# Kernel optimization log

Measured on AMD Instinct MI355X. Metric: run time of the kernel, lower is better.

The kernel has to match this reference:

```python
import jax, jax.numpy as jnp
import numpy as np

HH, WW = 56, 56          # input resolution
WS, SS = 7, 3            # window size, shift size
HEADS = 6
DIM = 192
HID = 768
B = 32
EPS = 1e-5


def _rel_pos_index(ws):
    coords = np.stack(np.meshgrid(np.arange(ws), np.arange(ws), indexing='ij'))  # [2,ws,ws]
    cf = coords.reshape(2, -1)                       # [2,N]
    rel = cf[:, :, None] - cf[:, None, :]            # [2,N,N]
    rel = rel.transpose(1, 2, 0).copy()              # [N,N,2]
    rel[:, :, 0] += ws - 1
    rel[:, :, 1] += ws - 1
    rel[:, :, 0] *= 2 * ws - 1
    return rel.sum(-1)                               # [N,N] int


def _attn_mask(H, W, ws, ss):
    img = np.zeros((H, W))
    cnt = 0
    sl = (slice(0, -ws), slice(-ws, -ss), slice(-ss, None))
    for hs in sl:
        for wsl in sl:
            img[hs, wsl] = cnt
            cnt += 1
    mw = img.reshape(H // ws, ws, W // ws, ws).transpose(0, 2, 1, 3).reshape(-1, ws * ws)  # [nW,N]
    diff = mw[:, None, :] - mw[:, :, None]           # matches unsqueeze(1)-unsqueeze(2)
    return np.where(diff != 0, -100.0, 0.0).astype(np.float32)  # [nW,N,N]


_RPI = jnp.asarray(_rel_pos_index(WS))               # [49,49] int
_MASK = jnp.asarray(_attn_mask(HH, WW, WS, SS))      # [64,49,49] f32


def _ln(v, g, b):
    mu = v.mean(-1, keepdims=True)
    var = v.var(-1, keepdims=True)
    return (v - mu) / jnp.sqrt(var + EPS) * g + b


def setup_inputs() -> dict:
    key = jax.random.key(0)
    ks = jax.random.split(key, 10)
    s = 0.02
    return {
        'x': jax.random.normal(ks[0], (B, HH * WW, DIM), jnp.float32),
        'norm1_g': jnp.ones((DIM,), jnp.float32),
        'norm1_b': jnp.zeros((DIM,), jnp.float32),
        'qkv_w': jax.random.normal(ks[1], (DIM, 3 * DIM), jnp.float32) * s,
        'qkv_b': jax.random.normal(ks[2], (3 * DIM,), jnp.float32) * s,
        'rpb_table': jax.random.normal(ks[3], (169, HEADS), jnp.float32) * s,
        'proj_w': jax.random.normal(ks[4], (DIM, DIM), jnp.float32) * s,
        'proj_b': jax.random.normal(ks[5], (DIM,), jnp.float32) * s,
        'norm2_g': jnp.ones((DIM,), jnp.float32),
        'norm2_b': jnp.zeros((DIM,), jnp.float32),
        'fc1_w': jax.random.normal(ks[6], (DIM, HID), jnp.float32) * s,
        'fc1_b': jax.random.normal(ks[7], (HID,), jnp.float32) * s,
        'fc2_w': jax.random.normal(ks[8], (HID, DIM), jnp.float32) * s,
        'fc2_b': jax.random.normal(ks[9], (DIM,), jnp.float32) * s,
    }


def reference(x, norm1_g, norm1_b, qkv_w, qkv_b, rpb_table, proj_w, proj_b,
              norm2_g, norm2_b, fc1_w, fc1_b, fc2_w, fc2_b):
    Bn, L, C = x.shape
    h, ws, ss = HEADS, WS, SS
    d = C // h
    scale = d ** -0.5
    N = ws * ws
    nWh, nWw = HH // ws, WW // ws

    shortcut = x
    xh = _ln(x, norm1_g, norm1_b).reshape(Bn, HH, WW, C)
    xh = jnp.roll(xh, (-ss, -ss), axis=(1, 2))                       # cyclic shift
    # window partition -> (B*nW, N, C)
    xw = xh.reshape(Bn, nWh, ws, nWw, ws, C).transpose(0, 1, 3, 2, 4, 5).reshape(-1, N, C)

    qkv = (xw @ qkv_w + qkv_b).reshape(-1, N, 3, h, d).transpose(2, 0, 3, 1, 4)
    q, k, v = qkv[0] * scale, qkv[1], qkv[2]                         # (B_,h,N,d)
    attn = jnp.einsum('bhnd,bhmd->bhnm', q, k)                       # (B_,h,N,N)

    bias = rpb_table[_RPI.reshape(-1)].reshape(N, N, h).transpose(2, 0, 1)  # (h,N,N)
    attn = attn + bias[None]
    nW = _MASK.shape[0]
    attn = attn.reshape(Bn, nW, h, N, N) + _MASK[None, :, None]
    attn = jax.nn.softmax(attn.reshape(-1, h, N, N), axis=-1)

    out = jnp.einsum('bhnm,bhmd->bhnd', attn, v).transpose(0, 2, 1, 3).reshape(-1, N, C)
    out = out @ proj_w + proj_b
    # window reverse
    out = out.reshape(Bn, nWh, nWw, ws, ws, C).transpose(0, 1, 3, 2, 4, 5).reshape(Bn, HH, WW, C)
    out = jnp.roll(out, (ss, ss), axis=(1, 2)).reshape(Bn, L, C)     # reverse shift

    x1 = shortcut + out
    y = _ln(x1, norm2_g, norm2_b)
    y = jax.nn.gelu(y @ fc1_w + fc1_b, approximate=False)
    y = y @ fc2_w + fc2_b
    return x1 + y
```

## Files before the change

### kernel.cpp

```cpp
#include <hip/hip_runtime.h>
#include <cmath>

typedef __bf16  v8bf  __attribute__((ext_vector_type(8)));
typedef float   v4f   __attribute__((ext_vector_type(4)));

#define HH 56
#define WW2 56
#define SS 3
#define HEADS 6
#define DIM 192
#define HID 768
#define NTOK 49
#define NWIN 2048
#define MTOT (NWIN * NTOK)
#define SCALE 0.17677669529663687f

__device__ __forceinline__ void async_cp16(const __bf16* g, __bf16* l) {
    __builtin_amdgcn_global_load_lds(
        (const __attribute__((address_space(1))) void*)g,
        (__attribute__((address_space(3))) void*)l,
        16, 0, 0);
}

__global__ void k_transpose(const float* __restrict__ in, __bf16* __restrict__ out,
                            int K, int N) {
    int idx = blockIdx.x * 256 + threadIdx.x;
    if (idx >= K * N) return;
    int n = idx / K, k = idx - n * K;
    out[idx] = (__bf16)in[k * N + n];
}

__global__ void k_prep_fc1(const float* __restrict__ w, __bf16* __restrict__ o) {
    int idx = blockIdx.x * 256 + threadIdx.x;
    if (idx >= HID * DIM) return;
    int n = idx / DIM, rem = idx - n * DIM;
    int b16 = rem >> 3, j = rem & 7;
    int k = 8 * (b16 ^ (n & 7)) + j;
    o[idx] = (__bf16)w[k * HID + n];
}

__global__ void k_prep_fc2(const float* __restrict__ w, __bf16* __restrict__ o) {
    int idx = blockIdx.x * 256 + threadIdx.x;
    if (idx >= HID * DIM) return;
    int hc = idx / (DIM * 64);
    int rem = idx - hc * DIM * 64;
    int n = rem >> 6;
    int rem2 = rem & 63;
    int b16 = rem2 >> 3, j = rem2 & 7;
    int k = hc * 64 + 8 * (b16 ^ (n & 7)) + j;
    o[idx] = (__bf16)w[k * DIM + n];
}

__global__ void k_bias(const float* __restrict__ rpb, float* __restrict__ bt) {
    int type = blockIdx.x, h = blockIdx.y;
    for (int idx = threadIdx.x; idx < 4096; idx += 256) {
        int m = idx >> 6, n = idx & 63;
        float v;
        if (m >= 49) v = -1e9f;
        else if (n >= 49) v = 0.f;
        else {
            int ni = n / 7, nj = n % 7, mi = m / 7, mj = m % 7;
            v = rpb[((ni - mi + 6) * 13 + (nj - mj + 6)) * 6 + h];
            int rin = (type & 2) ? ((ni < 4) ? 1 : 2) : 0;
            int rjn = (type & 1) ? ((nj < 4) ? 1 : 2) : 0;
            int rim = (type & 2) ? ((mi < 4) ? 1 : 2) : 0;
            int rjm = (type & 1) ? ((mj < 4) ? 1 : 2) : 0;
            if (rin * 3 + rjn != rim * 3 + rjm) v -= 100.f;
        }
        bt[((size_t)(type * HEADS + h) * 64 + m) * 64 + n] = v;
    }
}

__global__ __launch_bounds__(256) void k_ln1win(const float* __restrict__ x,
                                                const float* __restrict__ g,
                                                const float* __restrict__ bt,
                                                __bf16* __restrict__ xw) {
    int wv = threadIdx.x >> 6, lane = threadIdx.x & 63;
    int t = blockIdx.x * 4 + wv;
    int w = t / NTOK, p = t - w * NTOK;
    int b = w >> 6, wi = w & 63;
    int i = (wi >> 3) * 7 + p / 7;
    int j = (wi & 7) * 7 + p % 7;
    int io = i + SS; if (io >= HH) io -= HH;
    int jo = j + SS; if (jo >= WW2) jo -= WW2;
    const float* src = x + ((size_t)(b * 3136 + io * 56 + jo)) * DIM;
    float v0 = src[lane], v1 = src[lane + 64], v2 = src[lane + 128];
    float s = v0 + v1 + v2, s2 = v0 * v0 + v1 * v1 + v2 * v2;
    #pragma unroll
    for (int off = 1; off < 64; off <<= 1) {
        s  += __shfl_xor(s, off);
        s2 += __shfl_xor(s2, off);
    }
    float mu = s * (1.f / 192.f);
    float rstd = rsqrtf(s2 * (1.f / 192.f) - mu * mu + 1e-5f);
    __bf16* dst = xw + (size_t)t * DIM;
    dst[lane]       = (__bf16)((v0 - mu) * rstd * g[lane]       + bt[lane]);
    dst[lane + 64]  = (__bf16)((v1 - mu) * rstd * g[lane + 64]  + bt[lane + 64]);
    dst[lane + 128] = (__bf16)((v2 - mu) * rstd * g[lane + 128] + bt[lane + 128]);
}

template<int KDIM, int NDIM, int MODE>
__global__ __launch_bounds__(256) void k_gemm128(const __bf16* __restrict__ A,
                                                 const __bf16* __restrict__ Wt,
                                                 const float* __restrict__ bias,
                                                 __bf16* __restrict__ outb,
                                                 const float* __restrict__ x1in,
                                                 float* __restrict__ outf,
                                                 const float* __restrict__ xres) {
    __shared__ __bf16 lA[128 * 32];
    __shared__ __bf16 lB[128 * 32];
    const int tid = threadIdx.x;
    const int m0 = blockIdx.x * 128, n0 = blockIdx.y * 128;
    const int wv = tid >> 6, lane = tid & 63;
    const int wm = (wv >> 1) * 64, wn = (wv & 1) * 64;
    const int lrow = lane & 15, lq = lane >> 4;
    const int grow = tid >> 2, gkc = (tid & 3) * 8;
    v4f acc[4][4] = {};
    for (int kk = 0; kk < KDIM; kk += 32) {
        #pragma unroll
        for (int c = 0; c < 2; c++) {
            int r = grow + c * 64;
            async_cp16(A + (size_t)(m0 + r) * KDIM + kk + gkc, lA + tid * 8 + c * 2048);
            int rb = n0 + r;
            if (NDIM % 128) rb = (rb < NDIM) ? rb : (NDIM - 1);
            async_cp16(Wt + (size_t)rb * KDIM + kk + gkc, lB + tid * 8 + c * 2048);
        }
        __syncthreads();
        v8bf af[4], bf[4];
        #pragma unroll
        for (int i = 0; i < 4; i++) {
            af[i] = *(const v8bf*)(lA + (wm + i * 16 + lrow) * 32 + lq * 8);
            bf[i] = *(const v8bf*)(lB + (wn + i * 16 + lrow) * 32 + lq * 8);
        }
        #pragma unroll
        for (int i = 0; i < 4; i++)
        #pragma unroll
        for (int j = 0; j < 4; j++)
            acc[i][j] = __builtin_amdgcn_mfma_f32_16x16x32_bf16(af[i], bf[j], acc[i][j], 0, 0, 0);
        __syncthreads();
    }
    #pragma unroll
    for (int i = 0; i < 4; i++)
    #pragma unroll
    for (int j = 0; j < 4; j++) {
        int col = n0 + wn + j * 16 + lrow;
        if (NDIM % 128 && col >= NDIM) continue;
        float bv = bias[col];
        #pragma unroll
        for (int r = 0; r < 4; r++) {
            int row = m0 + wm + i * 16 + lq * 4 + r;
            float v = acc[i][j][r] + bv;
            if (MODE == 0) {
                __bf16* kbp = outb + (size_t)MTOT * DIM;
                __bf16* vbp = kbp + (size_t)MTOT * DIM;
                int which = col / DIM, rem = col - which * DIM;
                int hh = rem >> 5, d = rem & 31;
                int w = row / NTOK, p = row - w * NTOK;
                size_t off = ((size_t)(w * HEADS + hh) * NTOK + p) * 32 + d;
                if (which == 0)      outb[off] = (__bf16)(v * SCALE);
                else if (which == 1) kbp[off] = (__bf16)v;
                else                 vbp[off] = (__bf16)v;
            } else {
                int w = row / NTOK, p = row - w * NTOK;
                int bimg = w >> 6, wi = w & 63;
                int ii = (wi >> 3) * 7 + p / 7;
                int jj = (wi & 7) * 7 + p % 7;
                int io = ii + SS; if (io >= HH) io -= HH;
                int jo = jj + SS; if (jo >= WW2) jo -= WW2;
                size_t o = ((size_t)(bimg * 3136 + io * 56 + jo)) * DIM + col;
                outf[o] = v + xres[o];
            }
        }
    }
}

__global__ __launch_bounds__(64) void k_attn_mfma(const __bf16* __restrict__ qb,
                                                  const float* __restrict__ bias_tab,
                                                  __bf16* __restrict__ ao) {
    __shared__ __bf16 Pl[64 * 72];
    __shared__ __bf16 VTl[32 * 72];
    const __bf16* kb = qb + (size_t)MTOT * DIM;
    const __bf16* vb = kb + (size_t)MTOT * DIM;
    int wh = blockIdx.x;
    int w = wh / HEADS, h = wh - w * HEADS;
    int lane = threadIdx.x & 63;
    int c = lane & 15, q = lane >> 4;
    const size_t base = (size_t)wh * (NTOK * 32);

    for (int idx = lane; idx < 32 * 16; idx += 64)
        VTl[(idx >> 4) * 72 + 48 + (idx & 15)] = (__bf16)0.f;
    #pragma unroll
    for (int it = 0; it < 4; it++) {
        int idx = it * 64 + lane;
        if (idx < NTOK * 4) {
            int t = idx >> 2, d0 = (idx & 3) * 8;
            v8bf vv = *(const v8bf*)(vb + base + t * 32 + d0);
            #pragma unroll
            for (int ii = 0; ii < 8; ii++) VTl[(d0 + ii) * 72 + t] = vv[ii];
        }
    }
    v8bf af[4], bf[4];
    #pragma unroll
    for (int rt = 0; rt < 4; rt++) {
        int t = rt * 16 + c; t = (t > 48) ? 48 : t;
        af[rt] = *(const v8bf*)(qb + base + t * 32 + q * 8);
        bf[rt] = *(const v8bf*)(kb + base + t * 32 + q * 8);
    }
    v4f S[4][4] = {};
    #pragma unroll
    for (int rt = 0; rt < 4; rt++)
    #pragma unroll
    for (int ct = 0; ct < 4; ct++)
        S[rt][ct] = __builtin_amdgcn_mfma_f32_16x16x32_bf16(af[rt], bf[ct], S[rt][ct], 0, 0, 0);
    int wi = w & 63;
    int type = (((wi >> 3) == 7) ? 2 : 0) + (((wi & 7) == 7) ? 1 : 0);
    const float* bt = bias_tab + (size_t)(type * HEADS + h) * 4096;
    #pragma unroll
    for (int rt = 0; rt < 4; rt++)
    #pragma unroll
    for (int ct = 0; ct < 4; ct++) {
        v4f bv = *(const v4f*)(bt + (ct * 16 + c) * 64 + rt * 16 + q * 4);
        S[rt][ct] += bv;
    }
    v4f mx4[4], inv4[4];
    #pragma unroll
    for (int rt = 0; rt < 4; rt++) {
        v4f m;
        #pragma unroll
        for (int r = 0; r < 4; r++)
            m[r] = fmaxf(fmaxf(S[rt][0][r], S[rt][1][r]), fmaxf(S[rt][2][r], S[rt][3][r]));
        #pragma unroll
        for (int off = 1; off < 16; off <<= 1) {
            #pragma unroll
            for (int r = 0; r < 4; r++) m[r] = fmaxf(m[r], __shfl_xor(m[r], off));
        }
        mx4[rt] = m;
    }
    #pragma unroll
    for (int rt = 0; rt < 4; rt++) {
        v4f dsum = {};
        #pragma unroll
        for (int ct = 0; ct < 4; ct++) {
            #pragma unroll
            for (int r = 0; r < 4; r++) {
                float e = __expf(S[rt][ct][r] - mx4[rt][r]);
                dsum[r] += e;
                Pl[(rt * 16 + q * 4 + r) * 72 + ct * 16 + c] = (__bf16)e;
            }
        }
        #pragma unroll
        for (int off = 1; off < 16; off <<= 1) {
            #pragma unroll
            for (int r = 0; r < 4; r++) dsum[r] += __shfl_xor(dsum[r], off);
        }
        #pragma unroll
        for (int r = 0; r < 4; r++) inv4[rt][r] = 1.f / dsum[r];
    }
    __syncthreads();
    v4f O[4][2] = {};
    #pragma unroll
    for (int k2 = 0; k2 < 2; k2++) {
        v8bf pa[4], pb[2];
        #pragma unroll
        for (int rt = 0; rt < 4; rt++)
            pa[rt] = *(const v8bf*)(Pl + (rt * 16 + c) * 72 + k2 * 32 + q * 8);
        #pragma unroll
        for (int ct = 0; ct < 2; ct++)
            pb[ct] = *(const v8bf*)(VTl + (ct * 16 + c) * 72 + k2 * 32 + q * 8);
        #pragma unroll
        for (int rt = 0; rt < 4; rt++)
        #pragma unroll
        for (int ct = 0; ct < 2; ct++)
            O[rt][ct] = __builtin_amdgcn_mfma_f32_16x16x32_bf16(pa[rt], pb[ct], O[rt][ct], 0, 0, 0);
    }
    __bf16* aop = ao + (size_t)(w * NTOK) * DIM + h * 32;
    #pragma unroll
    for (int rt = 0; rt < 4; rt++)
    #pragma unroll
    for (int r = 0; r < 4; r++) {
        int row = rt * 16 + q * 4 + r;
        if (row < NTOK) {
            #pragma unroll
            for (int ct = 0; ct < 2; ct++)
                aop[(size_t)row * DIM + ct * 16 + c] = (__bf16)(O[rt][ct][r] * inv4[rt][r]);
        }
    }
}

__global__ __launch_bounds__(256, 2) void k_mlp_fused(
        const float* __restrict__ x1,
        const float* __restrict__ n2g, const float* __restrict__ n2b,
        const __bf16* __restrict__ fc1S, const float* __restrict__ fc1b,
        const __bf16* __restrict__ fc2S, const float* __restrict__ fc2b,
        float* __restrict__ out) {
    __shared__ __align__(16) char sm[57344];
    char* aT = sm;
    char* lW = sm + 24576;
    char* lH = sm + 49152;
    const int tid = threadIdx.x;
    const int wv = tid >> 6, lane = tid & 63;
    const int lrow = lane & 15, lq = lane >> 4;
    const int m0 = blockIdx.x * 64;

    #pragma unroll
    for (int p = 0; p < 6; ++p)
        async_cp16(fc1S + p * 2048 + tid * 8, (__bf16*)lW + p * 2048 + tid * 8);

    {
        float g0 = n2g[lane], g1 = n2g[lane + 64], g2 = n2g[lane + 128];
        float b0 = n2b[lane], b1 = n2b[lane + 64], b2 = n2b[lane + 128];
        #pragma unroll 4
        for (int it = 0; it < 16; ++it) {
            int row = wv * 16 + it;
            const float* src = x1 + (size_t)(m0 + row) * DIM;
            float v0 = src[lane], v1 = src[lane + 64], v2 = src[lane + 128];
            float s = v0 + v1 + v2, s2 = v0 * v0 + v1 * v1 + v2 * v2;
            #pragma unroll
            for (int off = 1; off < 64; off <<= 1) {
                s  += __shfl_xor(s, off);
                s2 += __shfl_xor(s2, off);
            }
            float mu = s * (1.f / 192.f);
            float rstd = rsqrtf(s2 * (1.f / 192.f) - mu * mu + 1e-5f);
            char* rb = aT + row * 384;
            int xo = (row & 7) << 4;
            *(__bf16*)(rb + ((lane * 2)       ^ xo)) = (__bf16)((v0 - mu) * rstd * g0 + b0);
            *(__bf16*)(rb + ((lane * 2 + 128) ^ xo)) = (__bf16)((v1 - mu) * rstd * g1 + b1);
            *(__bf16*)(rb + ((lane * 2 + 256) ^ xo)) = (__bf16)((v2 - mu) * rstd * g2 + b2);
        }
    }
    __syncthreads();

    const int wm = (wv >> 1) * 32;
    const int wc1 = (wv & 1) * 32;
    const int wn  = (wv & 1) * 96;
    v4f oacc[2][6] = {};

    for (int hc = 0; hc < 12; ++hc) {
        v4f hacc[2][2] = {};
        __builtin_amdgcn_s_setprio(1);
        #pragma unroll
        for (int ks = 0; ks < 6; ++ks) {
            v8bf af[2], bw[2];
            #pragma unroll
            for (int i = 0; i < 2; ++i) {
                int ra = wm + i * 16 + lrow;
                af[i] = *(const v8bf*)(aT + ra * 384 + ((ks * 64 + lq * 16) ^ ((ra & 7) << 4)));
                int rw = wc1 + i * 16 + lrow;
                bw[i] = *(const v8bf*)(lW + rw * 384 + ((ks * 64 + lq * 16) ^ ((rw & 7) << 4)));
            }
            #pragma unroll
            for (int i = 0; i < 2; ++i)
            #pragma unroll
            for (int j = 0; j < 2; ++j)
                hacc[i][j] = __builtin_amdgcn_mfma_f32_16x16x32_bf16(af[i], bw[j], hacc[i][j], 0, 0, 0);
        }
        __builtin_amdgcn_s_setprio(0);
        #pragma unroll
        for (int i = 0; i < 2; ++i)
        #pragma unroll
        for (int j = 0; j < 2; ++j) {
            float bv = fc1b[hc * 64 + wc1 + j * 16 + lrow];
            #pragma unroll
            for (int r = 0; r < 4; ++r) {
                int row = wm + i * 16 + lq * 4 + r;
                int col = wc1 + j * 16 + lrow;
                float hv = hacc[i][j][r] + bv;
                float ge = 0.5f * hv * (1.f + erff(hv * 0.70710678118654752f));
                *(__bf16*)(lH + row * 128 + ((col * 2) ^ ((row & 7) << 4))) = (__bf16)ge;
            }
        }
        __syncthreads();
        {
            const __bf16* src = fc2S + (size_t)hc * (192 * 64);
            #pragma unroll
            for (int p = 0; p < 6; ++p)
                async_cp16(src + p * 2048 + tid * 8, (__bf16*)lW + p * 2048 + tid * 8);
        }
        __syncthreads();
        __builtin_amdgcn_s_setprio(1);
        #pragma unroll
        for (int k2 = 0; k2 < 2; ++k2) {
            v8bf pa[2], pb[6];
            #pragma unroll
            for (int i = 0; i < 2; ++i) {
                int ra = wm + i * 16 + lrow;
                pa[i] = *(const v8bf*)(lH + ra * 128 + ((k2 * 64 + lq * 16) ^ ((ra & 7) << 4)));
            }
            #pragma unroll
            for (int j = 0; j < 6; ++j) {
                int rw = wn + j * 16 + lrow;
                pb[j] = *(const v8bf*)(lW + rw * 128 + ((k2 * 64 + lq * 16) ^ ((rw & 7) << 4)));
            }
            #pragma unroll
            for (int i = 0; i < 2; ++i)
            #pragma unroll
            for (int j = 0; j < 6; ++j)
                oacc[i][j] = __builtin_amdgcn_mfma_f32_16x16x32_bf16(pa[i], pb[j], oacc[i][j], 0, 0, 0);
        }
        __builtin_amdgcn_s_setprio(0);
        __syncthreads();
        if (hc < 11) {
            const __bf16* src = fc1S + (size_t)(hc + 1) * (64 * 192);
            #pragma unroll
            for (int p = 0; p < 6; ++p)
                async_cp16(src + p * 2048 + tid * 8, (__bf16*)lW + p * 2048 + tid * 8);
            __syncthreads();
        }
    }
    #pragma unroll
    for (int i = 0; i < 2; ++i)
    #pragma unroll
    for (int j = 0; j < 6; ++j) {
        int col = wn + j * 16 + lrow;
        float bv = fc2b[col];
        #pragma unroll
        for (int r = 0; r < 4; ++r) {
            int row = m0 + wm + i * 16 + lq * 4 + r;
            size_t o = (size_t)row * DIM + col;
            out[o] = oacc[i][j][r] + bv + x1[o];
        }
    }
}

extern "C" void kernel_launch(void* const* d_in, const int* in_sizes, int n_in,
                              void* d_out, int out_size, void* d_ws, size_t ws_size,
                              hipStream_t stream) {
    const float* x      = (const float*)d_in[0];
    const float* n1g    = (const float*)d_in[1];
    const float* n1b    = (const float*)d_in[2];
    const float* qkv_w  = (const float*)d_in[3];
    const float* qkv_b  = (const float*)d_in[4];
    const float* rpb    = (const float*)d_in[5];
    const float* proj_w = (const float*)d_in[6];
    const float* proj_b = (const float*)d_in[7];
    const float* n2g    = (const float*)d_in[8];
    const float* n2b    = (const float*)d_in[9];
    const float* fc1_w  = (const float*)d_in[10];
    const float* fc1_b  = (const float*)d_in[11];
    const float* fc2_w  = (const float*)d_in[12];
    const float* fc2_b  = (const float*)d_in[13];
    float* outp = (float*)d_out;

    char* ws = (char*)d_ws;
    const size_t SZA = (size_t)MTOT * DIM * 2;
    __bf16* xw = (__bf16*)ws;
    __bf16* qb = (__bf16*)(ws + SZA);
    float*  x1 = (float*)(ws + SZA);
    char* wbase = ws + 4 * SZA;
    __bf16* qkvT  = (__bf16*)wbase;
    __bf16* projT = qkvT + 576 * 192;
    __bf16* fc1S  = projT + 192 * 192;
    __bf16* fc2S  = fc1S + 768 * 192;
    float*  btab  = (float*)(fc2S + 768 * 192);

    k_transpose<<<(192 * 576 + 255) / 256, 256, 0, stream>>>(qkv_w, qkvT, 192, 576);
    k_transpose<<<(192 * 192 + 255) / 256, 256, 0, stream>>>(proj_w, projT, 192, 192);
    k_prep_fc1<<<(768 * 192 + 255) / 256, 256, 0, stream>>>(fc1_w, fc1S);
    k_prep_fc2<<<(768 * 192 + 255) / 256, 256, 0, stream>>>(fc2_w, fc2S);
    k_bias<<<dim3(4, HEADS), 256, 0, stream>>>(rpb, btab);

    k_ln1win<<<MTOT / 4, 256, 0, stream>>>(x, n1g, n1b, xw);

    k_gemm128<192, 576, 0><<<dim3(MTOT / 128, 5), 256, 0, stream>>>(
        xw, qkvT, qkv_b, qb, nullptr, nullptr, nullptr);

    k_attn_mfma<<<NWIN * HEADS, 64, 0, stream>>>(qb, btab, xw);

    k_gemm128<192, 192, 1><<<dim3(MTOT / 128, 2), 256, 0, stream>>>(
        xw, projT, proj_b, nullptr, nullptr, x1, x);

    k_mlp_fused<<<MTOT / 64, 256, 0, stream>>>(
        x1, n2g, n2b, fc1S, fc1_b, fc2S, fc2_b, outp);
}
```

Baseline: 524.0 us.

## Double-buffer fc1/fc2 weight tiles in MLP kernel with fine-grained waits and fast GELU

The fused MLP kernel now keeps the LayerNorm'd A operand in registers, which frees its LDS region to act as a second weight buffer. fc1 and fc2 weight chunks ping-pong between two buffers, and each next chunk is prefetched while the other GEMM runs. Block-wide __syncthreads are replaced by explicit vmcnt/lgkmcnt waits plus raw barriers. Biases are staged in LDS, and the erf-based GELU is replaced by a polynomial erf approximation. The approximation may change numerics slightly, and the manual waitcnt sequencing and extra registers risk hazards and lower occupancy.

```diff
diff --git a/kernel.cpp b/kernel.cpp
--- a/kernel.cpp
+++ b/kernel.cpp
@@ -20,6 +20,24 @@
         (const __attribute__((address_space(1))) void*)g,
         (__attribute__((address_space(3))) void*)l,
         16, 0, 0);
+}
+
+__device__ __forceinline__ void wg_barrier() {
+    __builtin_amdgcn_sched_barrier(0);
+    __builtin_amdgcn_s_barrier();
+    __builtin_amdgcn_sched_barrier(0);
+}
+#define WAIT_LGKM0() asm volatile("s_waitcnt lgkmcnt(0)" ::: "memory")
+#define WAIT_VM(n)   asm volatile("s_waitcnt vmcnt(" #n ")" ::: "memory")
+
+__device__ __forceinline__ float fast_gelu(float x) {
+    float z = fabsf(x) * 0.70710678118654752f;
+    float t = __builtin_amdgcn_rcpf(1.f + 0.3275911f * z);
+    float poly = t * (0.254829592f + t * (-0.284496736f +
+                 t * (1.421413741f + t * (-1.453152027f + t * 1.061405429f))));
+    float er = 1.f - poly * __expf(-z * z);
+    er = (x < 0.f) ? -er : er;
+    return 0.5f * x * (1.f + er);
 }
 
 __global__ void k_transpose(const float* __restrict__ in, __bf16* __restrict__ out,
@@ -293,10 +311,12 @@
         const __bf16* __restrict__ fc1S, const float* __restrict__ fc1b,
         const __bf16* __restrict__ fc2S, const float* __restrict__ fc2b,
         float* __restrict__ out) {
-    __shared__ __align__(16) char sm[57344];
-    char* aT = sm;
-    char* lW = sm + 24576;
-    char* lH = sm + 49152;
+    __shared__ __align__(16) char sm[61184];
+    char* bufX = sm;
+    char* bufY = sm + 24576;
+    char* lH   = sm + 49152;
+    float* lB1 = (float*)(sm + 57344);
+    float* lB2 = (float*)(sm + 60416);
     const int tid = threadIdx.x;
     const int wv = tid >> 6, lane = tid & 63;
     const int lrow = lane & 15, lq = lane >> 4;
@@ -304,7 +324,11 @@
 
     #pragma unroll
     for (int p = 0; p < 6; ++p)
-        async_cp16(fc1S + p * 2048 + tid * 8, (__bf16*)lW + p * 2048 + tid * 8);
+        async_cp16(fc1S + p * 2048 + tid * 8, (__bf16*)bufY + p * 2048 + tid * 8);
+
+    #pragma unroll
+    for (int p = 0; p < 3; ++p) lB1[p * 256 + tid] = fc1b[p * 256 + tid];
+    if (tid < 192) lB2[tid] = fc2b[tid];
 
     {
         float g0 = n2g[lane], g1 = n2g[lane + 64], g2 = n2g[lane + 128];
@@ -322,62 +346,77 @@
             }
             float mu = s * (1.f / 192.f);
             float rstd = rsqrtf(s2 * (1.f / 192.f) - mu * mu + 1e-5f);
-            char* rb = aT + row * 384;
+            char* rb = bufX + row * 384;
             int xo = (row & 7) << 4;
             *(__bf16*)(rb + ((lane * 2)       ^ xo)) = (__bf16)((v0 - mu) * rstd * g0 + b0);
             *(__bf16*)(rb + ((lane * 2 + 128) ^ xo)) = (__bf16)((v1 - mu) * rstd * g1 + b1);
             *(__bf16*)(rb + ((lane * 2 + 256) ^ xo)) = (__bf16)((v2 - mu) * rstd * g2 + b2);
         }
     }
-    __syncthreads();
-
-    const int wm = (wv >> 1) * 32;
+    WAIT_LGKM0();
+    wg_barrier();
+
+    const int wm  = (wv >> 1) * 32;
     const int wc1 = (wv & 1) * 32;
     const int wn  = (wv & 1) * 96;
+    v8bf afr[2][6];
+    #pragma unroll
+    for (int i = 0; i < 2; ++i) {
+        int ra = wm + i * 16 + lrow;
+        #pragma unroll
+        for (int ks = 0; ks < 6; ++ks)
+            afr[i][ks] = *(const v8bf*)(bufX + ra * 384 + ((ks * 64 + lq * 16) ^ ((ra & 7) << 4)));
+    }
+    WAIT_LGKM0();
+    wg_barrier();
+
+    #pragma unroll
+    for (int p = 0; p < 6; ++p)
+        async_cp16(fc2S + p * 2048 + tid * 8, (__bf16*)bufX + p * 2048 + tid * 8);
+
     v4f oacc[2][6] = {};
-
     for (int hc = 0; hc < 12; ++hc) {
+        int hn = hc + 1; if (hn == 12) hn = 0;
         v4f hacc[2][2] = {};
         __builtin_amdgcn_s_setprio(1);
         #pragma unroll
         for (int ks = 0; ks < 6; ++ks) {
-            v8bf af[2], bw[2];
-            #pragma unroll
-            for (int i = 0; i < 2; ++i) {
-                int ra = wm + i * 16 + lrow;
-                af[i] = *(const v8bf*)(aT + ra * 384 + ((ks * 64 + lq * 16) ^ ((ra & 7) << 4)));
-                int rw = wc1 + i * 16 + lrow;
-                bw[i] = *(const v8bf*)(lW + rw * 384 + ((ks * 64 + lq * 16) ^ ((rw & 7) << 4)));
+            v8bf bw[2];
+            #pragma unroll
+            for (int j = 0; j < 2; ++j) {
+                int rw = wc1 + j * 16 + lrow;
+                bw[j] = *(const v8bf*)(bufY + rw * 384 + ((ks * 64 + lq * 16) ^ ((rw & 7) << 4)));
             }
             #pragma unroll
             for (int i = 0; i < 2; ++i)
             #pragma unroll
             for (int j = 0; j < 2; ++j)
-                hacc[i][j] = __builtin_amdgcn_mfma_f32_16x16x32_bf16(af[i], bw[j], hacc[i][j], 0, 0, 0);
+                hacc[i][j] = __builtin_amdgcn_mfma_f32_16x16x32_bf16(afr[i][ks], bw[j], hacc[i][j], 0, 0, 0);
         }
         __builtin_amdgcn_s_setprio(0);
         #pragma unroll
         for (int i = 0; i < 2; ++i)
         #pragma unroll
         for (int j = 0; j < 2; ++j) {
-            float bv = fc1b[hc * 64 + wc1 + j * 16 + lrow];
+            float bv = lB1[hc * 64 + wc1 + j * 16 + lrow];
             #pragma unroll
             for (int r = 0; r < 4; ++r) {
                 int row = wm + i * 16 + lq * 4 + r;
                 int col = wc1 + j * 16 + lrow;
                 float hv = hacc[i][j][r] + bv;
-                float ge = 0.5f * hv * (1.f + erff(hv * 0.70710678118654752f));
-                *(__bf16*)(lH + row * 128 + ((col * 2) ^ ((row & 7) << 4))) = (__bf16)ge;
-            }
-        }
-        __syncthreads();
+                *(__bf16*)(lH + row * 128 + ((col * 2) ^ ((row & 7) << 4))) = (__bf16)fast_gelu(hv);
+            }
+        }
+        WAIT_LGKM0();
+        wg_barrier();
         {
-            const __bf16* src = fc2S + (size_t)hc * (192 * 64);
+            const __bf16* s1 = fc1S + (size_t)hn * (64 * 192);
             #pragma unroll
             for (int p = 0; p < 6; ++p)
-                async_cp16(src + p * 2048 + tid * 8, (__bf16*)lW + p * 2048 + tid * 8);
-        }
-        __syncthreads();
+                async_cp16(s1 + p * 2048 + tid * 8, (__bf16*)bufY + p * 2048 + tid * 8);
+        }
+        WAIT_VM(6);
+        wg_barrier();
         __builtin_amdgcn_s_setprio(1);
         #pragma unroll
         for (int k2 = 0; k2 < 2; ++k2) {
@@ -390,7 +429,7 @@
             #pragma unroll
             for (int j = 0; j < 6; ++j) {
                 int rw = wn + j * 16 + lrow;
-                pb[j] = *(const v8bf*)(lW + rw * 128 + ((k2 * 64 + lq * 16) ^ ((rw & 7) << 4)));
+                pb[j] = *(const v8bf*)(bufX + rw * 128 + ((k2 * 64 + lq * 16) ^ ((rw & 7) << 4)));
             }
             #pragma unroll
             for (int i = 0; i < 2; ++i)
@@ -399,21 +438,24 @@
                 oacc[i][j] = __builtin_amdgcn_mfma_f32_16x16x32_bf16(pa[i], pb[j], oacc[i][j], 0, 0, 0);
         }
         __builtin_amdgcn_s_setprio(0);
-        __syncthreads();
-        if (hc < 11) {
-            const __bf16* src = fc1S + (size_t)(hc + 1) * (64 * 192);
+        WAIT_LGKM0();
+        wg_barrier();
+        {
+            const __bf16* s2 = fc2S + (size_t)hn * (192 * 64);
             #pragma unroll
             for (int p = 0; p < 6; ++p)
-                async_cp16(src + p * 2048 + tid * 8, (__bf16*)lW + p * 2048 + tid * 8);
-            __syncthreads();
-        }
-    }
+                async_cp16(s2 + p * 2048 + tid * 8, (__bf16*)bufX + p * 2048 + tid * 8);
+        }
+        WAIT_VM(6);
+        wg_barrier();
+    }
+    WAIT_VM(0);
     #pragma unroll
     for (int i = 0; i < 2; ++i)
     #pragma unroll
     for (int j = 0; j < 6; ++j) {
         int col = wn + j * 16 + lrow;
-        float bv = fc2b[col];
+        float bv = lB2[col];
         #pragma unroll
         for (int r = 0; r < 4; ++r) {
             int row = m0 + wm + i * 16 + lq * 4 + r;
```

New measurement: 477.8 us. -8.8%, faster.
